# Kernel optimization log

Measured on AMD Instinct MI355X. Metric: run time of the kernel, lower is better.

## Reference

```python
import jax, jax.numpy as jnp
import numpy as np

B, T, F, U, D = 256, 2048, 37, 32, 16


def setup_inputs() -> dict:
    key = jax.random.key(0)
    ks = jax.random.split(key, 12)
    s = 0.05
    return {
        "demo": jax.random.normal(ks[0], (B, D), jnp.float32),
        "dt": jax.random.uniform(ks[1], (B, T, F), jnp.float32),
        "values": jax.random.normal(ks[2], (B, T, F), jnp.float32),
        "measurements": jax.random.randint(ks[3], (B, T, F), 0, 2, jnp.int32),
        "lengths": jax.random.randint(ks[4], (B,), 1, T + 1, jnp.int32),
        "W1": jax.random.normal(ks[5], (D, U), jnp.float32) * s,
        "b1": jnp.zeros((U,), jnp.float32),
        "W2": jax.random.normal(ks[6], (U, U), jnp.float32) * s,
        "b2": jnp.zeros((U,), jnp.float32),
        "kernel": jax.random.normal(ks[7], (3 * F, 3 * U), jnp.float32) * s,
        "rec_kernel": jax.random.normal(ks[8], (U, 3 * U), jnp.float32) * s,
        "bias": jnp.zeros((2, 3 * U), jnp.float32),
        "Wo": jax.random.normal(ks[9], (U, 1), jnp.float32) * s,
        "bo": jnp.zeros((1,), jnp.float32),
    }


def _gru_last(x, h0, kernel, rec_kernel, bias, mask):
    # x: [B,T,3F], h0: [B,U], mask: [B,T] bool. Keras GRU, reset_after=True,
    # gate order (z, r, h). Masked steps carry the previous state.
    b_in, b_rec = bias[0], bias[1]
    xz = x @ kernel + b_in                      # [B,T,3U], hoisted out of scan
    x_z, x_r, x_h = jnp.split(xz, 3, axis=-1)

    def step(h, inp):
        xz_t, xr_t, xh_t, m_t = inp
        rec = h @ rec_kernel + b_rec            # [B,3U]
        r_z, r_r, r_h = jnp.split(rec, 3, axis=-1)
        z = jax.nn.sigmoid(xz_t + r_z)
        r = jax.nn.sigmoid(xr_t + r_r)
        hh = jnp.tanh(xh_t + r * r_h)
        h_new = z * h + (1.0 - z) * hh
        h = jnp.where(m_t[:, None], h_new, h)
        return h, None

    inputs = (x_z.transpose(1, 0, 2), x_r.transpose(1, 0, 2),
              x_h.transpose(1, 0, 2), mask.T)
    h_last, _ = jax.lax.scan(step, h0, inputs)
    return h_last


def reference(demo, dt, values, measurements, lengths,
              W1, b1, W2, b2, kernel, rec_kernel, bias, Wo, bo):
    # demo encoder -> initial state
    h0 = jax.nn.relu(demo @ W1 + b1) @ W2 + b2                  # [B,U]
    # concat(values, measurements.float, dt) along features
    x = jnp.concatenate(
        (values, measurements.astype(jnp.float32), dt), axis=-1)  # [B,T,3F]
    mask = jnp.arange(x.shape[1])[None, :] < lengths[:, None]     # [B,T]
    h_last = _gru_last(x, h0, kernel, rec_kernel, bias, mask)
    return jax.nn.sigmoid(h_last @ Wo + bo)                       # [B,1]
```

## Files before the change

### kernel.cpp

```cpp
#include <hip/hip_runtime.h>

#define B_    256
#define T_    2048
#define F_    37
#define TF    111
#define U_    32
#define TU    96
#define D_    16

#define KP    128
#define XSTR  136
#define XZSTR 102
#define MTILE 128

#define L2E 1.4426950408889634f

typedef __attribute__((ext_vector_type(8))) short short8;
typedef __attribute__((ext_vector_type(4))) float f32x4;
typedef __attribute__((ext_vector_type(2))) float f32x2;

__device__ __forceinline__ float fast_exp2(float x) {
    float r; asm("v_exp_f32 %0, %1" : "=v"(r) : "v"(x)); return r;
}
__device__ __forceinline__ float fast_rcp(float x) {
    float r; asm("v_rcp_f32 %0, %1" : "=v"(r) : "v"(x)); return r;
}
__device__ __forceinline__ float sigmoid_fast(float x) {
    return fast_rcp(1.f + fast_exp2(-L2E * x));
}
__device__ __forceinline__ float rdlane(float v, int k) {
    return __uint_as_float(__builtin_amdgcn_readlane(__float_as_uint(v), k));
}
__device__ __forceinline__ float swap_half(float x) {
    unsigned xi = __float_as_uint(x);
    auto p = __builtin_amdgcn_permlane32_swap(xi, xi, false, false);
    float f0 = __uint_as_float(p[0]);
    float f1 = __uint_as_float(p[1]);
    return (f0 + f1) - x;
}
__device__ __forceinline__ float bf2f(unsigned short u) {
    return __uint_as_float(((unsigned)u) << 16);
}
__device__ __forceinline__ unsigned short f2bf_rne(float x) {
    unsigned u = __float_as_uint(x);
    return (unsigned short)((u + 0x7FFFu + ((u >> 16) & 1u)) >> 16);
}

#define PKMULV(d, hq, w) \
    asm("v_pk_mul_f32 %0, %1, %2" : "=v"(d) : "v"(hq), "v"(w))
#define PKFMAV(d, hq, w) \
    asm("v_pk_fma_f32 %0, %1, %2, %0" : "+v"(d) : "v"(hq), "v"(w))
#define PKADD(d, a, b) \
    asm("v_pk_add_f32 %0, %1, %2" : "=v"(d) : "v"(a), "v"(b))

#define SCHED_FENCE() __builtin_amdgcn_sched_barrier(0)
#define MEM_FENCE()   asm volatile("" ::: "memory")

__global__ __attribute__((amdgpu_flat_work_group_size(256, 256),
                          amdgpu_waves_per_eu(1, 1)))
void gru_pipe_kernel(
    const float* __restrict__ dt,
    const float* __restrict__ values,
    const int*   __restrict__ meas,
    const float* __restrict__ kern,
    const float* __restrict__ bias,
    const float* __restrict__ demo,
    const int*   __restrict__ lengths,
    const float* __restrict__ W1,
    const float* __restrict__ b1,
    const float* __restrict__ W2,
    const float* __restrict__ b2,
    const float* __restrict__ rec_kernel,
    const float* __restrict__ Wo,
    const float* __restrict__ bo,
    float* __restrict__ out)
{
    __shared__ unsigned short sX[MTILE][XSTR];
    __shared__ unsigned short sKT[TU][XSTR];
    __shared__ unsigned short sXZ[2][MTILE][XZSTR];
    __shared__ float sH[64];

    const int b    = blockIdx.x;
    const int tid  = threadIdx.x;
    const int wave = tid >> 6;
    const int lane = tid & 63;
    const int len  = lengths[b];
    const int ntiles = (len + MTILE - 1) / MTILE;
    const int lr   = lane & 15;
    const int lk   = (lane >> 4) * 8;

    for (int idx = tid; idx < TU * KP; idx += 256) {
        int k = idx / TU;
        int j = idx - k * TU;
        sKT[j][k] = (k < TF) ? f2bf_rne(kern[k * TU + j]) : (unsigned short)0;
    }
    for (int i = tid; i < MTILE * (KP - TF); i += 256) {
        int t = i / (KP - TF), p = i - t * (KP - TF);
        sX[t][TF + p] = 0;
    }
    __syncthreads();

    float bi[6];
    #pragma unroll
    for (int n = 0; n < 6; ++n) bi[n] = bias[n * 16 + lr];
    short8 bfr[6][4];
    #pragma unroll
    for (int n = 0; n < 6; ++n)
        #pragma unroll
        for (int kc = 0; kc < 4; ++kc)
            bfr[n][kc] = *(const short8*)&sKT[n * 16 + lr][kc * 32 + lk];

    auto mfma_chunk = [&](int c, int buf) {
        f32x4 acc[2][6];
        #pragma unroll
        for (int m = 0; m < 2; ++m)
            #pragma unroll
            for (int n = 0; n < 6; ++n) acc[m][n] = (f32x4){0.f, 0.f, 0.f, 0.f};
        #pragma unroll
        for (int kc = 0; kc < 4; ++kc) {
            short8 a0 = *(const short8*)&sX[c * 32 + lr][kc * 32 + lk];
            short8 a1 = *(const short8*)&sX[c * 32 + 16 + lr][kc * 32 + lk];
            #pragma unroll
            for (int n = 0; n < 6; ++n) {
                acc[0][n] = __builtin_amdgcn_mfma_f32_16x16x32_bf16(a0, bfr[n][kc], acc[0][n], 0, 0, 0);
                acc[1][n] = __builtin_amdgcn_mfma_f32_16x16x32_bf16(a1, bfr[n][kc], acc[1][n], 0, 0, 0);
            }
        }
        #pragma unroll
        for (int m = 0; m < 2; ++m)
            #pragma unroll
            for (int r = 0; r < 4; ++r) {
                int row = c * 32 + m * 16 + (lane >> 4) * 4 + r;
                #pragma unroll
                for (int n = 0; n < 6; ++n)
                    sXZ[buf][row][lr + n * 16] = f2bf_rne(acc[m][n][r] + bi[n]);
            }
    };

    for (int i = tid; i < MTILE * F_; i += 256) {
        int t = i / F_, f = i - t * F_;
        size_t g = ((size_t)b * T_ + t) * F_ + f;
        sX[t][f]          = f2bf_rne(values[g]);
        sX[t][F_ + f]     = meas[g] ? (unsigned short)0x3F80 : (unsigned short)0;
        sX[t][2 * F_ + f] = f2bf_rne(dt[g]);
    }
    __syncthreads();
    mfma_chunk(wave, 0);
    __syncthreads();

    if (wave != 0) {
        for (int k = 0; k < ntiles; ++k) {
            if (k + 1 < ntiles) {
                const int t0n = (k + 1) * MTILE;
                const int buf = (k + 1) & 1;
                const int nch = (wave == 1) ? 2 : 1;
                for (int ci = 0; ci < nch; ++ci) {
                    const int c = (wave == 1) ? (ci == 0 ? 0 : 3) : (wave - 1);
                    for (int i = lane; i < 32 * F_; i += 64) {
                        int tr = i / F_, f = i - tr * F_;
                        int t  = c * 32 + tr;
                        size_t g = ((size_t)b * T_ + (t0n + t)) * F_ + f;
                        sX[t][f]          = f2bf_rne(values[g]);
                        sX[t][F_ + f]     = meas[g] ? (unsigned short)0x3F80 : (unsigned short)0;
                        sX[t][2 * F_ + f] = f2bf_rne(dt[g]);
                    }
                    MEM_FENCE();
                    mfma_chunk(c, buf);
                }
            }
            __syncthreads();
        }
        return;
    }

    const int l   = lane;
    const int lc  = l & 31;
    const bool lower = (l < 32);

    f32x2 wpA[16], wpB[16];
    #pragma unroll
    for (int m = 0; m < 16; ++m) {
        wpA[m] = (f32x2){-L2E * rec_kernel[(2 * m) * TU + l],
                         -L2E * rec_kernel[(2 * m + 1) * TU + l]};
        wpB[m] = (f32x2){2.f * L2E * rec_kernel[(2 * m) * TU + 64 + lc],
                         2.f * L2E * rec_kernel[(2 * m + 1) * TU + 64 + lc]};
    }
    float rbA = -L2E * bias[TU + l];
    float rbB = 2.f * L2E * bias[TU + 64 + lc];
    #pragma unroll
    for (int m = 0; m < 16; ++m) {
        asm volatile("" : "+v"(wpA[m]));
        asm volatile("" : "+v"(wpB[m]));
    }
    asm volatile("" : "+v"(rbA), "+v"(rbB));

    float av = 0.f;
    if (l < U_) {
        float a = b1[l];
        #pragma unroll
        for (int d = 0; d < D_; ++d) a += demo[b * D_ + d] * W1[d * U_ + l];
        av = fmaxf(a, 0.f);
    }
    float hv = b2[lc];
    #pragma unroll
    for (int k = 0; k < U_; ++k) hv += rdlane(av, k) * W2[k * U_ + lc];

    typedef union { f32x4 q; f32x2 d[2]; } qd_u;
    unsigned short rA[4], rB[4];

    auto step = [&](float xApre, float xBpre) {
        sH[l] = hv;
        MEM_FENCE();
        qd_u hq[8];
        #pragma unroll
        for (int q = 0; q < 8; ++q)
            hq[q].q = *(const f32x4*)&sH[4 * q];
        MEM_FENCE();
        SCHED_FENCE();
        f32x2 aA0 = (f32x2){xApre, 0.f}, aA1, aA2, aA3;
        PKFMAV(aA0, hq[0].d[0], wpA[0]);
        PKMULV(aA1, hq[0].d[1], wpA[1]);
        PKMULV(aA2, hq[1].d[0], wpA[2]);
        PKMULV(aA3, hq[1].d[1], wpA[3]);
        #pragma unroll
        for (int g = 1; g < 4; ++g) {
            PKFMAV(aA0, hq[2 * g].d[0],     wpA[4 * g]);
            PKFMAV(aA1, hq[2 * g].d[1],     wpA[4 * g + 1]);
            PKFMAV(aA2, hq[2 * g + 1].d[0], wpA[4 * g + 2]);
            PKFMAV(aA3, hq[2 * g + 1].d[1], wpA[4 * g + 3]);
        }
        f32x2 tA01, tA23, tA;
        PKADD(tA01, aA0, aA1); PKADD(tA23, aA2, aA3); PKADD(tA, tA01, tA23);
        float recA = tA.x + tA.y;
        float eA = fast_exp2(recA);
        SCHED_FENCE();
        f32x2 aB0 = (f32x2){rbB, 0.f}, aB1, aB2, aB3;
        PKFMAV(aB0, hq[0].d[0], wpB[0]);
        PKMULV(aB1, hq[0].d[1], wpB[1]);
        PKMULV(aB2, hq[1].d[0], wpB[2]);
        PKMULV(aB3, hq[1].d[1], wpB[3]);
        PKFMAV(aB0, hq[2].d[0], wpB[4]);
        PKFMAV(aB1, hq[2].d[1], wpB[5]);
        PKFMAV(aB2, hq[3].d[0], wpB[6]);
        PKFMAV(aB3, hq[3].d[1], wpB[7]);
        SCHED_FENCE();
        float zr = fast_rcp(1.f + eA);
        SCHED_FENCE();
        #pragma unroll
        for (int g = 2; g < 4; ++g) {
            PKFMAV(aB0, hq[2 * g].d[0],     wpB[4 * g]);
            PKFMAV(aB1, hq[2 * g].d[1],     wpB[4 * g + 1]);
            PKFMAV(aB2, hq[2 * g + 1].d[0], wpB[4 * g + 2]);
            PKFMAV(aB3, hq[2 * g + 1].d[1], wpB[4 * g + 3]);
        }
        f32x2 tB01, tB23, tB;
        PKADD(tB01, aB0, aB1); PKADD(tB23, aB2, aB3); PKADD(tB, tB01, tB23);
        float recB = tB.x + tB.y;
        SCHED_FENCE();
        float sw = swap_half(zr);
        float z  = lower ? zr : sw;
        float r  = lower ? sw : zr;
        float u2 = fmaf(r, recB, xBpre);
        float e2 = fast_exp2(u2);
        float hh = fmaf(-2.f, fast_rcp(e2 + 1.f), 1.f);
        hv = fmaf(z, hv - hh, hh);
    };

    for (int k = 0; k < ntiles; ++k) {
        const int t0    = k * MTILE;
        const int left  = len - t0;
        const int steps = (left < MTILE) ? left : MTILE;
        const unsigned short* xb = &sXZ[k & 1][0][0];

        auto rd4 = [&](int i0) {
            #pragma unroll
            for (int i = 0; i < 4; ++i) {
                int ii = i0 + i; ii = (ii < steps) ? ii : (steps - 1);
                rA[i] = xb[ii * XZSTR + l];
                rB[i] = xb[ii * XZSTR + 64 + lc];
            }
        };

        rd4(0);
        const int fullt = steps & ~3;
        for (int ig = 0; ig < fullt; ig += 4) {
            float pA0 = fmaf(bf2f(rA[0]), -L2E, rbA), pB0 = bf2f(rB[0]) * (2.f * L2E);
            float pA1 = fmaf(bf2f(rA[1]), -L2E, rbA), pB1 = bf2f(rB[1]) * (2.f * L2E);
            float pA2 = fmaf(bf2f(rA[2]), -L2E, rbA), pB2 = bf2f(rB[2]) * (2.f * L2E);
            float pA3 = fmaf(bf2f(rA[3]), -L2E, rbA), pB3 = bf2f(rB[3]) * (2.f * L2E);
            rd4(ig + 4);
            step(pA0, pB0); step(pA1, pB1); step(pA2, pB2); step(pA3, pB3);
        }
        const int rem = steps - fullt;
        if (rem > 0) step(fmaf(bf2f(rA[0]), -L2E, rbA), bf2f(rB[0]) * (2.f * L2E));
        if (rem > 1) step(fmaf(bf2f(rA[1]), -L2E, rbA), bf2f(rB[1]) * (2.f * L2E));
        if (rem > 2) step(fmaf(bf2f(rA[2]), -L2E, rbA), bf2f(rB[2]) * (2.f * L2E));

        __syncthreads();
    }

    float v = (l < U_) ? hv * Wo[l] : 0.f;
    v += __shfl_xor(v, 16);
    v += __shfl_xor(v, 8);
    v += __shfl_xor(v, 4);
    v += __shfl_xor(v, 2);
    v += __shfl_xor(v, 1);
    if (l == 0) out[b] = sigmoid_fast(v + bo[0]);
}

extern "C" void kernel_launch(void* const* d_in, const int* in_sizes, int n_in,
                              void* d_out, int out_size, void* d_ws, size_t ws_size,
                              hipStream_t stream) {
    const float* demo       = (const float*)d_in[0];
    const float* dt         = (const float*)d_in[1];
    const float* values     = (const float*)d_in[2];
    const int*   meas       = (const int*)  d_in[3];
    const int*   lengths    = (const int*)  d_in[4];
    const float* W1         = (const float*)d_in[5];
    const float* b1         = (const float*)d_in[6];
    const float* W2         = (const float*)d_in[7];
    const float* b2         = (const float*)d_in[8];
    const float* kern       = (const float*)d_in[9];
    const float* rec_kernel = (const float*)d_in[10];
    const float* bias       = (const float*)d_in[11];
    const float* Wo         = (const float*)d_in[12];
    const float* bo         = (const float*)d_in[13];
    float* out = (float*)d_out;

    hipLaunchKernelGGL(gru_pipe_kernel, dim3(B_), dim3(256), 0, stream,
                       dt, values, meas, kern, bias, demo, lengths,
                       W1, b1, W2, b2, rec_kernel, Wo, bo, out);
}
```

Measured before the change: 428.2 us.

## Transpose gate-input buffer and pack bf16 conversions in staging and MFMA epilogue

Stores the precomputed input-projection tile time-major per gate column ([96][132] instead of [128][102]). The recurrent wave can then fetch four consecutive timesteps with one 8-byte LDS load per gate instead of eight scalar 2-byte loads. The MFMA epilogue writes packed bf16 pairs via v_cvt_pk_bf16_f32, and input staging converts feature pairs with packed stores. The odd feature count is handled through a shifted column mapping for the meas block. This cuts LDS instruction count on the serial critical path and in the producer waves. The mapping is intricate and risks misaligned or out-of-range reads past the valid steps in the final tile, since the old clamp on the step index is gone.

Measured after the change: 393.5 us, median of 2. 8.1% less time.

```diff
diff --git a/kernel.cpp b/kernel.cpp
--- a/kernel.cpp
+++ b/kernel.cpp
@@ -10,14 +10,16 @@
 
 #define KP    128
 #define XSTR  136
-#define XZSTR 102
+#define TSTR  132
 #define MTILE 128
 
 #define L2E 1.4426950408889634f
 
 typedef __attribute__((ext_vector_type(8))) short short8;
+typedef __attribute__((ext_vector_type(4))) short s16x4;
 typedef __attribute__((ext_vector_type(4))) float f32x4;
 typedef __attribute__((ext_vector_type(2))) float f32x2;
+typedef __attribute__((ext_vector_type(2))) unsigned uint2v;
 
 __device__ __forceinline__ float fast_exp2(float x) {
     float r; asm("v_exp_f32 %0, %1" : "=v"(r) : "v"(x)); return r;
@@ -45,6 +47,11 @@
     unsigned u = __float_as_uint(x);
     return (unsigned short)((u + 0x7FFFu + ((u >> 16) & 1u)) >> 16);
 }
+__device__ __forceinline__ unsigned pk_bf16(float a, float b) {
+    unsigned u;
+    asm("v_cvt_pk_bf16_f32 %0, %1, %2" : "=v"(u) : "v"(a), "v"(b));
+    return u;
+}
 
 #define PKMULV(d, hq, w) \
     asm("v_pk_mul_f32 %0, %1, %2" : "=v"(d) : "v"(hq), "v"(w))
@@ -58,7 +65,7 @@
 
 __global__ __attribute__((amdgpu_flat_work_group_size(256, 256),
                           amdgpu_waves_per_eu(1, 1)))
-void gru_pipe_kernel(
+void gru_pipe2_kernel(
     const float* __restrict__ dt,
     const float* __restrict__ values,
     const int*   __restrict__ meas,
@@ -77,7 +84,7 @@
 {
     __shared__ unsigned short sX[MTILE][XSTR];
     __shared__ unsigned short sKT[TU][XSTR];
-    __shared__ unsigned short sXZ[2][MTILE][XZSTR];
+    __shared__ unsigned short sXZ[2][TU][TSTR];
     __shared__ float sH[64];
 
     const int b    = blockIdx.x;
@@ -110,6 +117,28 @@
         for (int kc = 0; kc < 4; ++kc)
             bfr[n][kc] = *(const short8*)&sKT[n * 16 + lr][kc * 32 + lk];
 
+    auto stage_chunk = [&](int c, int t0) {
+        for (int i = lane; i < 32 * 18; i += 64) {
+            int tr = i / 18, p = i - tr * 18;
+            int t = c * 32 + tr;
+            size_t g = ((size_t)b * T_ + (t0 + t)) * F_;
+            *(unsigned*)&sX[t][2 * p] =
+                pk_bf16(values[g + 2 * p], values[g + 2 * p + 1]);
+            *(unsigned*)&sX[t][38 + 2 * p] =
+                pk_bf16(meas[g + 1 + 2 * p] ? 1.f : 0.f,
+                        meas[g + 2 + 2 * p] ? 1.f : 0.f);
+            *(unsigned*)&sX[t][74 + 2 * p] =
+                pk_bf16(dt[g + 2 * p], dt[g + 2 * p + 1]);
+        }
+        if (lane < 32) {
+            int t = c * 32 + lane;
+            size_t g = ((size_t)b * T_ + (t0 + t)) * F_;
+            *(unsigned*)&sX[t][36] =
+                pk_bf16(values[g + 36], meas[g] ? 1.f : 0.f);
+            *(unsigned*)&sX[t][110] = pk_bf16(dt[g + 36], 0.f);
+        }
+    };
+
     auto mfma_chunk = [&](int c, int buf) {
         f32x4 acc[2][6];
         #pragma unroll
@@ -127,24 +156,19 @@
             }
         }
         #pragma unroll
-        for (int m = 0; m < 2; ++m)
+        for (int m = 0; m < 2; ++m) {
+            const int tb = c * 32 + m * 16 + (lane >> 4) * 4;
             #pragma unroll
-            for (int r = 0; r < 4; ++r) {
-                int row = c * 32 + m * 16 + (lane >> 4) * 4 + r;
-                #pragma unroll
-                for (int n = 0; n < 6; ++n)
-                    sXZ[buf][row][lr + n * 16] = f2bf_rne(acc[m][n][r] + bi[n]);
+            for (int n = 0; n < 6; ++n) {
+                unsigned lo = pk_bf16(acc[m][n][0] + bi[n], acc[m][n][1] + bi[n]);
+                unsigned hi = pk_bf16(acc[m][n][2] + bi[n], acc[m][n][3] + bi[n]);
+                *(uint2v*)&sXZ[buf][lr + n * 16][tb] = (uint2v){lo, hi};
             }
+        }
     };
 
-    for (int i = tid; i < MTILE * F_; i += 256) {
-        int t = i / F_, f = i - t * F_;
-        size_t g = ((size_t)b * T_ + t) * F_ + f;
-        sX[t][f]          = f2bf_rne(values[g]);
-        sX[t][F_ + f]     = meas[g] ? (unsigned short)0x3F80 : (unsigned short)0;
-        sX[t][2 * F_ + f] = f2bf_rne(dt[g]);
-    }
-    __syncthreads();
+    stage_chunk(wave, 0);
+    MEM_FENCE();
     mfma_chunk(wave, 0);
     __syncthreads();
 
@@ -156,14 +180,7 @@
                 const int nch = (wave == 1) ? 2 : 1;
                 for (int ci = 0; ci < nch; ++ci) {
                     const int c = (wave == 1) ? (ci == 0 ? 0 : 3) : (wave - 1);
-                    for (int i = lane; i < 32 * F_; i += 64) {
-                        int tr = i / F_, f = i - tr * F_;
-                        int t  = c * 32 + tr;
-                        size_t g = ((size_t)b * T_ + (t0n + t)) * F_ + f;
-                        sX[t][f]          = f2bf_rne(values[g]);
-                        sX[t][F_ + f]     = meas[g] ? (unsigned short)0x3F80 : (unsigned short)0;
-                        sX[t][2 * F_ + f] = f2bf_rne(dt[g]);
-                    }
+                    stage_chunk(c, t0n);
                     MEM_FENCE();
                     mfma_chunk(c, buf);
                 }
@@ -206,7 +223,7 @@
     for (int k = 0; k < U_; ++k) hv += rdlane(av, k) * W2[k * U_ + lc];
 
     typedef union { f32x4 q; f32x2 d[2]; } qd_u;
-    unsigned short rA[4], rB[4];
+    typedef union { s16x4 v; unsigned short u[4]; } s4u;
 
     auto step = [&](float xApre, float xBpre) {
         sH[l] = hv;
@@ -267,34 +284,30 @@
     };
 
     for (int k = 0; k < ntiles; ++k) {
-        const int t0    = k * MTILE;
-        const int left  = len - t0;
+        const int left  = len - k * MTILE;
         const int steps = (left < MTILE) ? left : MTILE;
-        const unsigned short* xb = &sXZ[k & 1][0][0];
-
+        const int kb    = k & 1;
+
+        s4u a4, b4;
         auto rd4 = [&](int i0) {
-            #pragma unroll
-            for (int i = 0; i < 4; ++i) {
-                int ii = i0 + i; ii = (ii < steps) ? ii : (steps - 1);
-                rA[i] = xb[ii * XZSTR + l];
-                rB[i] = xb[ii * XZSTR + 64 + lc];
-            }
+            a4.v = *(const s16x4*)&sXZ[kb][l][i0];
+            b4.v = *(const s16x4*)&sXZ[kb][64 + lc][i0];
         };
 
         rd4(0);
         const int fullt = steps & ~3;
         for (int ig = 0; ig < fullt; ig += 4) {
-            float pA0 = fmaf(bf2f(rA[0]), -L2E, rbA), pB0 = bf2f(rB[0]) * (2.f * L2E);
-            float pA1 = fmaf(bf2f(rA[1]), -L2E, rbA), pB1 = bf2f(rB[1]) * (2.f * L2E);
-            float pA2 = fmaf(bf2f(rA[2]), -L2E, rbA), pB2 = bf2f(rB[2]) * (2.f * L2E);
-            float pA3 = fmaf(bf2f(rA[3]), -L2E, rbA), pB3 = bf2f(rB[3]) * (2.f * L2E);
+            float pA0 = fmaf(bf2f(a4.u[0]), -L2E, rbA), pB0 = bf2f(b4.u[0]) * (2.f * L2E);
+            float pA1 = fmaf(bf2f(a4.u[1]), -L2E, rbA), pB1 = bf2f(b4.u[1]) * (2.f * L2E);
+            float pA2 = fmaf(bf2f(a4.u[2]), -L2E, rbA), pB2 = bf2f(b4.u[2]) * (2.f * L2E);
+            float pA3 = fmaf(bf2f(a4.u[3]), -L2E, rbA), pB3 = bf2f(b4.u[3]) * (2.f * L2E);
             rd4(ig + 4);
             step(pA0, pB0); step(pA1, pB1); step(pA2, pB2); step(pA3, pB3);
         }
         const int rem = steps - fullt;
-        if (rem > 0) step(fmaf(bf2f(rA[0]), -L2E, rbA), bf2f(rB[0]) * (2.f * L2E));
-        if (rem > 1) step(fmaf(bf2f(rA[1]), -L2E, rbA), bf2f(rB[1]) * (2.f * L2E));
-        if (rem > 2) step(fmaf(bf2f(rA[2]), -L2E, rbA), bf2f(rB[2]) * (2.f * L2E));
+        if (rem > 0) step(fmaf(bf2f(a4.u[0]), -L2E, rbA), bf2f(b4.u[0]) * (2.f * L2E));
+        if (rem > 1) step(fmaf(bf2f(a4.u[1]), -L2E, rbA), bf2f(b4.u[1]) * (2.f * L2E));
+        if (rem > 2) step(fmaf(bf2f(a4.u[2]), -L2E, rbA), bf2f(b4.u[2]) * (2.f * L2E));
 
         __syncthreads();
     }
@@ -327,7 +340,7 @@
     const float* bo         = (const float*)d_in[13];
     float* out = (float*)d_out;
 
-    hipLaunchKernelGGL(gru_pipe_kernel, dim3(B_), dim3(256), 0, stream,
+    hipLaunchKernelGGL(gru_pipe2_kernel, dim3(B_), dim3(256), 0, stream,
                        dt, values, meas, kern, bias, demo, lengths,
                        W1, b1, W2, b2, rec_kernel, Wo, bo, out);
 }
```
